# Performance work log

Hardware: AMD Instinct MI355X
Metric: run time of the kernel (lower is better)

The kernel has to match this reference:

```python
import jax, jax.numpy as jnp
import numpy as np

N_NODES = 50000
N_EDGES = 600000
IN_FEAT = 128
OUT_FEAT = 128
NUM_RELS = 8


def setup_inputs() -> dict:
    key = jax.random.key(0)
    ks = jax.random.split(key, 8)
    h = jax.random.normal(ks[0], (N_NODES, IN_FEAT), dtype=jnp.float32)
    # xavier_uniform-like scale for relation weights
    limit = float(np.sqrt(6.0 / (IN_FEAT + OUT_FEAT)))
    weight = jax.random.uniform(ks[1], (NUM_RELS, IN_FEAT, OUT_FEAT), jnp.float32, -limit, limit)
    limit_g = float(np.sqrt(6.0 / (IN_FEAT + 1)))
    gate_weight = jax.random.uniform(ks[2], (NUM_RELS, IN_FEAT, 1), jnp.float32, -limit_g, limit_g)
    h_bias = jnp.zeros((OUT_FEAT,), jnp.float32)
    loop_weight = jax.random.uniform(ks[3], (IN_FEAT, OUT_FEAT), jnp.float32, -limit, limit)
    norm = jax.random.uniform(ks[4], (N_EDGES, 1), jnp.float32)
    src = jax.random.randint(ks[5], (N_EDGES,), 0, N_NODES, dtype=jnp.int32)
    dst = jax.random.randint(ks[6], (N_EDGES,), 0, N_NODES, dtype=jnp.int32)
    rel_type = jax.random.randint(ks[7], (N_EDGES,), 0, NUM_RELS, dtype=jnp.int32)
    return {"h": h, "weight": weight, "gate_weight": gate_weight, "h_bias": h_bias,
            "loop_weight": loop_weight, "norm": norm, "src": src, "dst": dst,
            "rel_type": rel_type}


def reference(h, weight, gate_weight, h_bias, loop_weight, norm, src, dst, rel_type):
    n_nodes = h.shape[0]
    # Transform all nodes under every relation once ([R, N, out]); cheaper than
    # materializing per-edge [E, in, out] weight gathers for small R.
    h_rel = jnp.einsum('ni,rio->rno', h, weight)          # [R, N, out]
    msg = h_rel[rel_type, src]                             # [E, out] gather
    msg = msg * norm                                       # per-edge norm
    # relation-specific scalar gate on src features
    gate_rel = jnp.einsum('ni,ri->rn', h, gate_weight[:, :, 0])  # [R, N]
    gate = jax.nn.sigmoid(gate_rel[rel_type, src])[:, None]      # [E, 1]
    msg = msg * gate
    # scatter-sum messages into destination nodes
    agg = jax.ops.segment_sum(msg, dst, num_segments=n_nodes)    # [N, out]
    out = agg + h_bias + h @ loop_weight                   # bias + self-loop
    out = jax.nn.relu(out)                                 # activation
    # dropout p=0.0 (deterministic) -> identity
    return out
```

## Files before the change

### kernel.cpp

```cpp
#include <hip/hip_runtime.h>

#define N_NODES 50000
#define N_EDGES 600000
#define F 128
#define NBIN 400000
#define NBS1 1563

#define WT_OFF   0
#define H2_OFF   294912
#define GATE_OFF 13094912
#define CNT_OFF  14694912
#define EXCL_OFF 16295424
#define BSUM_OFF 17895936
#define REC_OFF  17902336
#define WS_NEED  ((size_t)22702336)

#define LDA 136

typedef __attribute__((ext_vector_type(8))) short short8;
typedef __attribute__((ext_vector_type(4))) float floatx4;

__device__ inline unsigned short f32_to_bf16(float f) {
    unsigned u = __float_as_uint(f);
    unsigned r = u + 0x7fff + ((u >> 16) & 1);
    return (unsigned short)(r >> 16);
}
__device__ inline float bf16lo(unsigned m) { return __uint_as_float(m << 16); }
__device__ inline float bf16hi(unsigned m) { return __uint_as_float(m & 0xffff0000u); }
__device__ inline float sigmoidf(float x) { return 1.f / (1.f + __expf(-x)); }

__global__ void k_prep_w(const float* __restrict__ W, const float* __restrict__ LW,
                         unsigned short* __restrict__ Wt) {
    int idx = blockIdx.x * 256 + threadIdx.x;
    if (idx >= 9 * 128 * 128) return;
    int r = idx >> 14;
    int rem = idx & 16383;
    int i = rem >> 7, o = rem & 127;
    float v = (r < 8) ? W[(r << 14) + (i << 7) + o] : LW[(i << 7) + o];
    Wt[(r << 14) + (o << 7) + i] = f32_to_bf16(v);
}

__global__ void k_prep(const float* __restrict__ h, const float* __restrict__ gw,
                       const int* __restrict__ dst, const int* __restrict__ rel,
                       unsigned short* __restrict__ h2, float* __restrict__ gate,
                       int* __restrict__ cnt) {
    int e = blockIdx.x * 256 + threadIdx.x;
    if (e < N_EDGES) atomicAdd(&cnt[rel[e] * N_NODES + dst[e]], 1);

    int wave = threadIdx.x >> 6, lane = threadIdx.x & 63;
    int n = blockIdx.x * 4 + wave;
    float2 hv = *(const float2*)(h + (size_t)n * F + lane * 2);
    unsigned val = (unsigned)f32_to_bf16(hv.x) | ((unsigned)f32_to_bf16(hv.y) << 16);
    *(unsigned*)(h2 + (size_t)n * F + lane * 2) = val;
    #pragma unroll
    for (int r = 0; r < 8; ++r) {
        float2 wv = *(const float2*)(gw + r * F + lane * 2);
        float p = hv.x * wv.x + hv.y * wv.y;
        #pragma unroll
        for (int off = 32; off; off >>= 1) p += __shfl_xor(p, off);
        if (lane == 0) gate[r * N_NODES + n] = sigmoidf(p);
    }
}

__global__ void k_s1(const int* __restrict__ cnt, int* __restrict__ excl,
                     int* __restrict__ bsum) {
    __shared__ int wsum[4];
    int g = blockIdx.x * 256 + threadIdx.x;
    int wave = threadIdx.x >> 6, lane = threadIdx.x & 63;
    int v = (g < NBIN) ? cnt[g] : 0;
    int x = v;
    #pragma unroll
    for (int off = 1; off < 64; off <<= 1) {
        int t = __shfl_up(x, off);
        if (lane >= off) x += t;
    }
    if (lane == 63) wsum[wave] = x;
    __syncthreads();
    int pre = 0;
    #pragma unroll
    for (int w = 0; w < 4; ++w) if (w < wave) pre += wsum[w];
    if (g < NBIN) excl[g] = x + pre - v;
    if (threadIdx.x == 255) bsum[blockIdx.x] = x + pre;
}

__global__ void k_s2(int* __restrict__ bsum) {
    __shared__ int sh[256];
    int t = threadIdx.x;
    int v[7];
    int s = 0;
    #pragma unroll
    for (int j = 0; j < 7; ++j) {
        int idx = t * 7 + j;
        v[j] = (idx < NBS1) ? bsum[idx] : 0;
        s += v[j];
    }
    sh[t] = s;
    __syncthreads();
    #pragma unroll
    for (int off = 1; off < 256; off <<= 1) {
        int tt = (t >= off) ? sh[t - off] : 0;
        __syncthreads();
        sh[t] += tt;
        __syncthreads();
    }
    int run = sh[t] - s;
    #pragma unroll
    for (int j = 0; j < 7; ++j) {
        int idx = t * 7 + j;
        if (idx < NBS1) bsum[idx] = run;
        run += v[j];
    }
}

__global__ void k_scatter(const int* __restrict__ src, const int* __restrict__ dst,
                          const int* __restrict__ rel, const float* __restrict__ norm,
                          const float* __restrict__ gate,
                          const int* __restrict__ excl, const int* __restrict__ bsum,
                          int* __restrict__ cnt, int2* __restrict__ rec) {
    int e = blockIdx.x * 256 + threadIdx.x;
    if (e >= N_EDGES) return;
    int d = dst[e], r = rel[e], s = src[e];
    int bin = r * N_NODES + d;
    int base = excl[bin] + bsum[bin >> 8];
    int old = atomicSub(&cnt[bin], 1);
    float sc = norm[e] * gate[r * N_NODES + s];
    rec[base + old - 1] = make_int2(s, __float_as_int(sc));
}

__global__ __launch_bounds__(1024, 8) void k_fused(const unsigned short* __restrict__ h2,
                                                   const unsigned short* __restrict__ Wt,
                                                   const int2* __restrict__ rec,
                                                   const int* __restrict__ excl,
                                                   const int* __restrict__ bsum,
                                                   const float* __restrict__ bias,
                                                   float* __restrict__ out) {
    __shared__ unsigned short sA[64 * LDA];
    __shared__ unsigned short sB[128 * LDA];
    int tid = threadIdx.x;
    int w = tid >> 6, lane = tid & 63;
    int lrow = lane & 15, quad = lane >> 4;
    int nb = blockIdx.x * 64;
    int mblk = w >> 2;
    int nblk = w & 3;

    floatx4 acc[2];
    acc[0] = (floatx4){0.f, 0.f, 0.f, 0.f};
    acc[1] = (floatx4){0.f, 0.f, 0.f, 0.f};

    for (int kb = 0; kb < 9; ++kb) {
        __syncthreads();
        #pragma unroll
        for (int it = 0; it < 2; ++it) {
            int G = it * 1024 + tid;
            int row = G >> 4, gr = G & 15;
            *(uint4*)(&sB[row * LDA + gr * 8]) = *(const uint4*)(Wt + (kb << 14) + G * 8);
        }
        if (kb < 8) {
            int b = 0;
            if (lane < 5) {
                int node = nb + w * 4 + lane;
                int nd = (node < N_NODES) ? node : N_NODES;
                int eff = kb * N_NODES + nd;
                b = (eff < NBIN) ? (excl[eff] + bsum[eff >> 8]) : N_EDGES;
            }
            int b0 = __shfl(b, 0);
            int degT = __shfl(b, 4) - b0;
            int rs = 0, rscl = 0;
            if (lane < degT) {
                int2 rc = rec[b0 + lane];
                rs = rc.x; rscl = rc.y;
            }
            #pragma unroll
            for (int rr = 0; rr < 4; ++rr) {
                int s = __shfl(b, rr), e = __shfl(b, rr + 1);
                float a0 = 0.f, a1 = 0.f;
                for (int j = s; j < e; ++j) {
                    int off = j - b0;
                    int sj; float sc;
                    if (off < 64) {
                        sj = __shfl(rs, off);
                        sc = __int_as_float(__shfl(rscl, off));
                    } else {
                        int2 rc = rec[j];
                        sj = rc.x; sc = __int_as_float(rc.y);
                    }
                    unsigned m = *(const unsigned*)(h2 + (size_t)sj * F + lane * 2);
                    a0 += sc * bf16lo(m);
                    a1 += sc * bf16hi(m);
                }
                int row = w * 4 + rr;
                unsigned val = (unsigned)f32_to_bf16(a0) | ((unsigned)f32_to_bf16(a1) << 16);
                ((unsigned*)sA)[row * (LDA / 2) + lane] = val;
            }
        } else {
            int row = tid >> 4, gr = tid & 15;
            int node = nb + row;
            uint4 v;
            if (node < N_NODES) v = *(const uint4*)(h2 + (size_t)node * F + gr * 8);
            else { v.x = 0; v.y = 0; v.z = 0; v.w = 0; }
            *(uint4*)(&sA[row * LDA + gr * 8]) = v;
        }
        __syncthreads();
        #pragma unroll
        for (int kt = 0; kt < 4; ++kt) {
            short8 a = *(const short8*)(&sA[(mblk * 16 + lrow) * LDA + kt * 32 + quad * 8]);
            #pragma unroll
            for (int nt = 0; nt < 2; ++nt) {
                short8 bb = *(const short8*)(&sB[(nblk * 32 + nt * 16 + lrow) * LDA + kt * 32 + quad * 8]);
                acc[nt] = __builtin_amdgcn_mfma_f32_16x16x32_bf16(a, bb, acc[nt], 0, 0, 0);
            }
        }
    }
    #pragma unroll
    for (int nt = 0; nt < 2; ++nt) {
        int col = nblk * 32 + nt * 16 + lrow;
        float bv = bias[col];
        #pragma unroll
        for (int g = 0; g < 4; ++g) {
            int row = nb + mblk * 16 + quad * 4 + g;
            if (row < N_NODES)
                out[(size_t)row * F + col] = fmaxf(acc[nt][g] + bv, 0.f);
        }
    }
}

__global__ void k_edges_fb(const float* __restrict__ h, const float* __restrict__ W,
                           const float* __restrict__ gw, const float* __restrict__ norm,
                           const int* __restrict__ src, const int* __restrict__ dst,
                           const int* __restrict__ rel, float* __restrict__ out) {
    int wave = threadIdx.x >> 6, lane = threadIdx.x & 63;
    int e = blockIdx.x * 4 + wave;
    if (e >= N_EDGES) return;
    int s = src[e], d = dst[e], r = rel[e];
    float2 hv = *(const float2*)(h + (size_t)s * F + lane * 2);
    float2 gv = *(const float2*)(gw + r * F + lane * 2);
    float p = hv.x * gv.x + hv.y * gv.y;
    #pragma unroll
    for (int off = 32; off; off >>= 1) p += __shfl_xor(p, off);
    float scale = norm[e] * sigmoidf(p);
    const float* wr = W + ((size_t)r << 14);
    float a0 = 0.f, a1 = 0.f;
    for (int i2 = 0; i2 < 64; ++i2) {
        float x0 = __shfl(hv.x, i2), x1 = __shfl(hv.y, i2);
        a0 += x0 * wr[(2 * i2) * F + lane]      + x1 * wr[(2 * i2 + 1) * F + lane];
        a1 += x0 * wr[(2 * i2) * F + 64 + lane] + x1 * wr[(2 * i2 + 1) * F + 64 + lane];
    }
    unsafeAtomicAdd(out + (size_t)d * F + lane,      a0 * scale);
    unsafeAtomicAdd(out + (size_t)d * F + 64 + lane, a1 * scale);
}

__global__ void k_final_fb(const float* __restrict__ h, const float* __restrict__ LW,
                           const float* __restrict__ bias, float* __restrict__ out) {
    int wave = threadIdx.x >> 6, lane = threadIdx.x & 63;
    int n = blockIdx.x * 4 + wave;
    if (n >= N_NODES) return;
    float2 hv = *(const float2*)(h + (size_t)n * F + lane * 2);
    float a0 = 0.f, a1 = 0.f;
    for (int i2 = 0; i2 < 64; ++i2) {
        float x0 = __shfl(hv.x, i2), x1 = __shfl(hv.y, i2);
        a0 += x0 * LW[(2 * i2) * F + lane]      + x1 * LW[(2 * i2 + 1) * F + lane];
        a1 += x0 * LW[(2 * i2) * F + 64 + lane] + x1 * LW[(2 * i2 + 1) * F + 64 + lane];
    }
    float* op = out + (size_t)n * F;
    op[lane]      = fmaxf(op[lane]      + bias[lane]      + a0, 0.f);
    op[64 + lane] = fmaxf(op[64 + lane] + bias[64 + lane] + a1, 0.f);
}

extern "C" void kernel_launch(void* const* d_in, const int* in_sizes, int n_in,
                              void* d_out, int out_size, void* d_ws, size_t ws_size,
                              hipStream_t stream) {
    const float* h    = (const float*)d_in[0];
    const float* W    = (const float*)d_in[1];
    const float* gw   = (const float*)d_in[2];
    const float* bias = (const float*)d_in[3];
    const float* lw   = (const float*)d_in[4];
    const float* norm = (const float*)d_in[5];
    const int* src    = (const int*)d_in[6];
    const int* dst    = (const int*)d_in[7];
    const int* rel    = (const int*)d_in[8];
    float* out = (float*)d_out;

    if (ws_size >= WS_NEED) {
        unsigned short* Wt   = (unsigned short*)((char*)d_ws + WT_OFF);
        unsigned short* h2   = (unsigned short*)((char*)d_ws + H2_OFF);
        float*          gate = (float*)((char*)d_ws + GATE_OFF);
        int*            cnt  = (int*)((char*)d_ws + CNT_OFF);
        int*            excl = (int*)((char*)d_ws + EXCL_OFF);
        int*            bsum = (int*)((char*)d_ws + BSUM_OFF);
        int2*           rec  = (int2*)((char*)d_ws + REC_OFF);

        hipMemsetAsync(cnt, 0, 400128 * sizeof(int), stream);
        k_prep_w<<<576, 256, 0, stream>>>(W, lw, Wt);
        k_prep<<<12500, 256, 0, stream>>>(h, gw, dst, rel, h2, gate, cnt);
        k_s1<<<NBS1, 256, 0, stream>>>(cnt, excl, bsum);
        k_s2<<<1, 256, 0, stream>>>(bsum);
        k_scatter<<<2344, 256, 0, stream>>>(src, dst, rel, norm, gate, excl, bsum, cnt, rec);
        k_fused<<<782, 1024, 0, stream>>>(h2, Wt, rec, excl, bsum, bias, out);
    } else {
        hipMemsetAsync(d_out, 0, (size_t)out_size * sizeof(float), stream);
        k_edges_fb<<<150000, 256, 0, stream>>>(h, W, gw, norm, src, dst, rel, out);
        k_final_fb<<<12500, 256, 0, stream>>>(h, lw, bias, out);
    }
}
```

Measured before the change: 291.9 us.

## Bin edges by destination only and select relation per k-step via ballot

Replaces the (relation, destination) CSR with a destination-only CSR. Relation ids are packed into the upper bits of the source index, and each k-block picks its relation's edges with a ballot mask over edge records held in registers and loaded once. This shrinks the counting and scan work: the two-level scan over 400k bins becomes a single-block scan over 50k nodes. It also folds the weight-prep kernel into the prep kernel, removing launches. The risks are a serial single-block scan, per-relation ballot work repeated across nine k steps, and source ids packed into 16 bits. N_NODES is 50000, so that packing only works because it fits under 65536.

```diff
diff --git a/kernel.cpp b/kernel.cpp
--- a/kernel.cpp
+++ b/kernel.cpp
@@ -3,17 +3,15 @@
 #define N_NODES 50000
 #define N_EDGES 600000
 #define F 128
-#define NBIN 400000
-#define NBS1 1563
 
 #define WT_OFF   0
 #define H2_OFF   294912
 #define GATE_OFF 13094912
 #define CNT_OFF  14694912
-#define EXCL_OFF 16295424
-#define BSUM_OFF 17895936
-#define REC_OFF  17902336
-#define WS_NEED  ((size_t)22702336)
+#define BASE_OFF 14894976
+#define CUR_OFF  15095040
+#define REC_OFF  15295104
+#define WS_NEED  ((size_t)20095104)
 
 #define LDA 136
 
@@ -29,24 +27,18 @@
 __device__ inline float bf16hi(unsigned m) { return __uint_as_float(m & 0xffff0000u); }
 __device__ inline float sigmoidf(float x) { return 1.f / (1.f + __expf(-x)); }
 
-__global__ void k_prep_w(const float* __restrict__ W, const float* __restrict__ LW,
-                         unsigned short* __restrict__ Wt) {
-    int idx = blockIdx.x * 256 + threadIdx.x;
-    if (idx >= 9 * 128 * 128) return;
-    int r = idx >> 14;
-    int rem = idx & 16383;
-    int i = rem >> 7, o = rem & 127;
-    float v = (r < 8) ? W[(r << 14) + (i << 7) + o] : LW[(i << 7) + o];
-    Wt[(r << 14) + (o << 7) + i] = f32_to_bf16(v);
-}
-
 __global__ void k_prep(const float* __restrict__ h, const float* __restrict__ gw,
-                       const int* __restrict__ dst, const int* __restrict__ rel,
+                       const float* __restrict__ W, const float* __restrict__ LW,
+                       const int* __restrict__ dst,
                        unsigned short* __restrict__ h2, float* __restrict__ gate,
-                       int* __restrict__ cnt) {
-    int e = blockIdx.x * 256 + threadIdx.x;
-    if (e < N_EDGES) atomicAdd(&cnt[rel[e] * N_NODES + dst[e]], 1);
-
+                       unsigned short* __restrict__ Wt, int* __restrict__ cnt) {
+    int gid = blockIdx.x * 256 + threadIdx.x;
+    if (gid < N_EDGES) atomicAdd(&cnt[dst[gid]], 1);
+    if (gid < 9 * 128 * 128) {
+        int r = gid >> 14, rem = gid & 16383, i = rem >> 7, o = rem & 127;
+        float v = (r < 8) ? W[(r << 14) + (i << 7) + o] : LW[(i << 7) + o];
+        Wt[(r << 14) + (o << 7) + i] = f32_to_bf16(v);
+    }
     int wave = threadIdx.x >> 6, lane = threadIdx.x & 63;
     int n = blockIdx.x * 4 + wave;
     float2 hv = *(const float2*)(h + (size_t)n * F + lane * 2);
@@ -62,76 +54,66 @@
     }
 }
 
-__global__ void k_s1(const int* __restrict__ cnt, int* __restrict__ excl,
-                     int* __restrict__ bsum) {
-    __shared__ int wsum[4];
-    int g = blockIdx.x * 256 + threadIdx.x;
-    int wave = threadIdx.x >> 6, lane = threadIdx.x & 63;
-    int v = (g < NBIN) ? cnt[g] : 0;
-    int x = v;
+__global__ __launch_bounds__(1024) void k_scan(const int* __restrict__ cnt,
+                                               int* __restrict__ base,
+                                               int* __restrict__ cursor) {
+    __shared__ int wpart[16];
+    const int CH = 49;
+    int t = threadIdx.x, lane = t & 63, w = t >> 6;
+    int st = t * CH;
+    int s = 0;
+    for (int i = 0; i < CH; ++i) {
+        int idx = st + i;
+        if (idx < N_NODES) s += cnt[idx];
+    }
+    int x = s;
     #pragma unroll
     for (int off = 1; off < 64; off <<= 1) {
-        int t = __shfl_up(x, off);
-        if (lane >= off) x += t;
-    }
-    if (lane == 63) wsum[wave] = x;
+        int tt = __shfl_up(x, off);
+        if (lane >= off) x += tt;
+    }
+    if (lane == 63) wpart[w] = x;
     __syncthreads();
-    int pre = 0;
-    #pragma unroll
-    for (int w = 0; w < 4; ++w) if (w < wave) pre += wsum[w];
-    if (g < NBIN) excl[g] = x + pre - v;
-    if (threadIdx.x == 255) bsum[blockIdx.x] = x + pre;
-}
-
-__global__ void k_s2(int* __restrict__ bsum) {
-    __shared__ int sh[256];
-    int t = threadIdx.x;
-    int v[7];
-    int s = 0;
-    #pragma unroll
-    for (int j = 0; j < 7; ++j) {
-        int idx = t * 7 + j;
-        v[j] = (idx < NBS1) ? bsum[idx] : 0;
-        s += v[j];
-    }
-    sh[t] = s;
+    if (t < 16) {
+        int y = wpart[t];
+        #pragma unroll
+        for (int off = 1; off < 16; off <<= 1) {
+            int tt = __shfl_up(y, off);
+            if (t >= off) y += tt;
+        }
+        wpart[t] = y;
+    }
     __syncthreads();
-    #pragma unroll
-    for (int off = 1; off < 256; off <<= 1) {
-        int tt = (t >= off) ? sh[t - off] : 0;
-        __syncthreads();
-        sh[t] += tt;
-        __syncthreads();
-    }
-    int run = sh[t] - s;
-    #pragma unroll
-    for (int j = 0; j < 7; ++j) {
-        int idx = t * 7 + j;
-        if (idx < NBS1) bsum[idx] = run;
-        run += v[j];
-    }
+    int pre = (w > 0) ? wpart[w - 1] : 0;
+    int run = pre + x - s;
+    for (int i = 0; i < CH; ++i) {
+        int idx = st + i;
+        if (idx < N_NODES) {
+            int v = cnt[idx];
+            base[idx] = run;
+            cursor[idx] = run;
+            run += v;
+        }
+    }
+    if (t == 0) base[N_NODES] = N_EDGES;
 }
 
 __global__ void k_scatter(const int* __restrict__ src, const int* __restrict__ dst,
                           const int* __restrict__ rel, const float* __restrict__ norm,
                           const float* __restrict__ gate,
-                          const int* __restrict__ excl, const int* __restrict__ bsum,
-                          int* __restrict__ cnt, int2* __restrict__ rec) {
+                          int* __restrict__ cursor, int2* __restrict__ rec) {
     int e = blockIdx.x * 256 + threadIdx.x;
     if (e >= N_EDGES) return;
     int d = dst[e], r = rel[e], s = src[e];
-    int bin = r * N_NODES + d;
-    int base = excl[bin] + bsum[bin >> 8];
-    int old = atomicSub(&cnt[bin], 1);
+    int pos = atomicAdd(&cursor[d], 1);
     float sc = norm[e] * gate[r * N_NODES + s];
-    rec[base + old - 1] = make_int2(s, __float_as_int(sc));
-}
-
-__global__ __launch_bounds__(1024, 8) void k_fused(const unsigned short* __restrict__ h2,
+    rec[pos] = make_int2(s | (r << 16), __float_as_int(sc));
+}
+
+__global__ __launch_bounds__(1024, 2) void k_fused(const unsigned short* __restrict__ h2,
                                                    const unsigned short* __restrict__ Wt,
                                                    const int2* __restrict__ rec,
-                                                   const int* __restrict__ excl,
-                                                   const int* __restrict__ bsum,
+                                                   const int* __restrict__ base,
                                                    const float* __restrict__ bias,
                                                    float* __restrict__ out) {
     __shared__ unsigned short sA[64 * LDA];
@@ -140,8 +122,28 @@
     int w = tid >> 6, lane = tid & 63;
     int lrow = lane & 15, quad = lane >> 4;
     int nb = blockIdx.x * 64;
-    int mblk = w >> 2;
-    int nblk = w & 3;
+    int mblk = w >> 2, nblk = w & 3;
+    int n0 = nb + w * 4;
+
+    int b = N_EDGES;
+    if (lane < 5) {
+        int idx = n0 + lane;
+        if (idx > N_NODES) idx = N_NODES;
+        b = base[idx];
+    }
+    int b0 = __shfl(b, 0), b1 = __shfl(b, 1), b2 = __shfl(b, 2);
+    int b3 = __shfl(b, 3), b4 = __shfl(b, 4);
+    int degT = b4 - b0;
+    int nreg = degT < 64 ? degT : 64;
+    int srcrel = 0, scl = 0;
+    if (lane < nreg) {
+        int2 rc = rec[b0 + lane];
+        srcrel = rc.x; scl = rc.y;
+    }
+    int idxa = b0 + lane;
+    int rowid = (idxa >= b1) + (idxa >= b2) + (idxa >= b3);
+    int myrel = (srcrel >> 16) & 7;
+    bool valid = lane < nreg;
 
     floatx4 acc[2];
     acc[0] = (floatx4){0.f, 0.f, 0.f, 0.f};
@@ -156,37 +158,41 @@
             *(uint4*)(&sB[row * LDA + gr * 8]) = *(const uint4*)(Wt + (kb << 14) + G * 8);
         }
         if (kb < 8) {
-            int b = 0;
-            if (lane < 5) {
-                int node = nb + w * 4 + lane;
-                int nd = (node < N_NODES) ? node : N_NODES;
-                int eff = kb * N_NODES + nd;
-                b = (eff < NBIN) ? (excl[eff] + bsum[eff >> 8]) : N_EDGES;
-            }
-            int b0 = __shfl(b, 0);
-            int degT = __shfl(b, 4) - b0;
-            int rs = 0, rscl = 0;
-            if (lane < degT) {
-                int2 rc = rec[b0 + lane];
-                rs = rc.x; rscl = rc.y;
-            }
             #pragma unroll
             for (int rr = 0; rr < 4; ++rr) {
-                int s = __shfl(b, rr), e = __shfl(b, rr + 1);
+                unsigned long long m = __ballot(valid && rowid == rr && myrel == kb);
                 float a0 = 0.f, a1 = 0.f;
-                for (int j = s; j < e; ++j) {
-                    int off = j - b0;
-                    int sj; float sc;
-                    if (off < 64) {
-                        sj = __shfl(rs, off);
-                        sc = __int_as_float(__shfl(rscl, off));
-                    } else {
+                if (m) {
+                    int j = __ffsll(m) - 1; m &= m - 1;
+                    float sc = __int_as_float(__shfl(scl, j));
+                    int sj = __shfl(srcrel, j) & 0xffff;
+                    unsigned mv = *(const unsigned*)(h2 + (size_t)sj * F + lane * 2);
+                    while (m) {
+                        int j2 = __ffsll(m) - 1; m &= m - 1;
+                        float sc2 = __int_as_float(__shfl(scl, j2));
+                        int sj2 = __shfl(srcrel, j2) & 0xffff;
+                        unsigned mv2 = *(const unsigned*)(h2 + (size_t)sj2 * F + lane * 2);
+                        a0 += sc * bf16lo(mv);
+                        a1 += sc * bf16hi(mv);
+                        sc = sc2; mv = mv2;
+                    }
+                    a0 += sc * bf16lo(mv);
+                    a1 += sc * bf16hi(mv);
+                }
+                if (degT > 64) {
+                    int brr  = (rr == 0) ? b0 : ((rr == 1) ? b1 : ((rr == 2) ? b2 : b3));
+                    int brr1 = (rr == 0) ? b1 : ((rr == 1) ? b2 : ((rr == 2) ? b3 : b4));
+                    int jlo = b0 + 64 > brr ? b0 + 64 : brr;
+                    for (int j = jlo; j < brr1; ++j) {
                         int2 rc = rec[j];
-                        sj = rc.x; sc = __int_as_float(rc.y);
+                        if (((rc.x >> 16) & 7) == kb) {
+                            float sc = __int_as_float(rc.y);
+                            int sj = rc.x & 0xffff;
+                            unsigned mv = *(const unsigned*)(h2 + (size_t)sj * F + lane * 2);
+                            a0 += sc * bf16lo(mv);
+                            a1 += sc * bf16hi(mv);
+                        }
                     }
-                    unsigned m = *(const unsigned*)(h2 + (size_t)sj * F + lane * 2);
-                    a0 += sc * bf16lo(m);
-                    a1 += sc * bf16hi(m);
                 }
                 int row = w * 4 + rr;
                 unsigned val = (unsigned)f32_to_bf16(a0) | ((unsigned)f32_to_bf16(a1) << 16);
@@ -285,17 +291,15 @@
         unsigned short* h2   = (unsigned short*)((char*)d_ws + H2_OFF);
         float*          gate = (float*)((char*)d_ws + GATE_OFF);
         int*            cnt  = (int*)((char*)d_ws + CNT_OFF);
-        int*            excl = (int*)((char*)d_ws + EXCL_OFF);
-        int*            bsum = (int*)((char*)d_ws + BSUM_OFF);
+        int*            base = (int*)((char*)d_ws + BASE_OFF);
+        int*            cur  = (int*)((char*)d_ws + CUR_OFF);
         int2*           rec  = (int2*)((char*)d_ws + REC_OFF);
 
-        hipMemsetAsync(cnt, 0, 400128 * sizeof(int), stream);
-        k_prep_w<<<576, 256, 0, stream>>>(W, lw, Wt);
-        k_prep<<<12500, 256, 0, stream>>>(h, gw, dst, rel, h2, gate, cnt);
-        k_s1<<<NBS1, 256, 0, stream>>>(cnt, excl, bsum);
-        k_s2<<<1, 256, 0, stream>>>(bsum);
-        k_scatter<<<2344, 256, 0, stream>>>(src, dst, rel, norm, gate, excl, bsum, cnt, rec);
-        k_fused<<<782, 1024, 0, stream>>>(h2, Wt, rec, excl, bsum, bias, out);
+        hipMemsetAsync(cnt, 0, N_NODES * sizeof(int), stream);
+        k_prep<<<12500, 256, 0, stream>>>(h, gw, W, lw, dst, h2, gate, Wt, cnt);
+        k_scan<<<1, 1024, 0, stream>>>(cnt, base, cur);
+        k_scatter<<<2344, 256, 0, stream>>>(src, dst, rel, norm, gate, cur, rec);
+        k_fused<<<782, 1024, 0, stream>>>(h2, Wt, rec, base, bias, out);
     } else {
         hipMemsetAsync(d_out, 0, (size_t)out_size * sizeof(float), stream);
         k_edges_fb<<<150000, 256, 0, stream>>>(h, W, gw, norm, src, dst, rel, out);
```

New measurement: 446.5 us. +53.0%, slower.
